# Performance work log

Hardware: AMD Instinct MI355X
Metric: run time of the kernel (lower is better)

## Reference

```python
import jax, jax.numpy as jnp
import numpy as np

DT = 1e-3   # timestep (s)
DH = 10.0   # grid spacing (m)


def setup_inputs() -> dict:
    key = jax.random.key(0)
    k1, k2, k3, k4 = jax.random.split(key, 4)
    B, NT, NZ, NX, NREC = 8, 256, 256, 256, 64
    x = jax.random.normal(k1, (B, NT), dtype=jnp.float32)            # source wavelets
    vp = 1500.0 + 2000.0 * jax.random.uniform(k2, (NZ, NX), dtype=jnp.float32)
    src_loc = jax.random.randint(k3, (B, 2), 4, NZ - 4, dtype=jnp.int32)        # (z,x) per shot
    rec_loc = jax.random.randint(k4, (B, NREC, 2), 4, NZ - 4, dtype=jnp.int32)  # (z,x) per rec
    return {"x": x, "vp": vp, "src_loc": src_loc, "rec_loc": rec_loc}


def reference(x, vp, src_loc, rec_loc):
    """Acoustic 2nd-order leapfrog FD time-stepping (WaveRNN pattern):
    per step: stencil update -> source scatter-inject -> receiver gather.
    Returns receiver traces (B, NT, NREC)."""
    B, NT = x.shape
    nz, nx = vp.shape
    c2dt2 = (vp * vp) * jnp.float32(DT * DT)   # (nz, nx), broadcast over batch
    inv_dh2 = jnp.float32(1.0 / (DH * DH))
    bidx = jnp.arange(B)
    sz, sx = src_loc[:, 0], src_loc[:, 1]
    rz, rx = rec_loc[..., 0], rec_loc[..., 1]

    def laplacian(h):  # 5-point stencil, zero (Dirichlet) boundaries
        interior = (h[:, 2:, 1:-1] + h[:, :-2, 1:-1]
                    + h[:, 1:-1, 2:] + h[:, 1:-1, :-2]
                    - 4.0 * h[:, 1:-1, 1:-1]) * inv_dh2
        return jnp.zeros_like(h).at[:, 1:-1, 1:-1].set(interior)

    def step(carry, wav_t):
        h1, h2 = carry                              # fields at t, t-1
        hn = 2.0 * h1 - h2 + c2dt2 * laplacian(h1)  # leapfrog update
        hn = hn.at[bidx, sz, sx].add(jnp.float32(DT * DT) * wav_t)  # source inject
        rec = hn[bidx[:, None], rz, rx]             # receiver gather (B, NREC)
        return (hn, h1), rec

    h0 = jnp.zeros((B, nz, nx), dtype=x.dtype)
    _, recs = jax.lax.scan(step, (h0, h0), x.T)     # recs: (NT, B, NREC)
    return jnp.transpose(recs, (1, 0, 2))           # (B, NT, NREC)
```

## Files before the change

kernel.cpp:

```cpp
#include <hip/hip_runtime.h>

typedef float v4f __attribute__((ext_vector_type(4)));

namespace {
constexpr int B_     = 8;
constexpr int NT_    = 256;
constexpr int NX_    = 256;
constexpr int NREC_  = 64;
constexpr int PIECES = 32;
constexpr int IROWS  = 8;
constexpr int G      = 16;
constexpr int ROUNDS = NT_ / G;
constexpr int NB     = (IROWS + 2 * G) / 4;
constexpr int NTHR   = NB * 64;
constexpr int NBLK   = B_ * PIECES;
constexpr float DT2  = 1e-6f;
constexpr float KLAP = 1e-8f;
constexpr size_t FLAGS_BYTES = 4096;
constexpr int RCAP = 6;
}

__device__ __forceinline__ float dpp_shr1(float v) {
    return __int_as_float(__builtin_amdgcn_update_dpp(
        0, __float_as_int(v), 0x138 , 0xF, 0xF, true));
}
__device__ __forceinline__ float dpp_shl1(float v) {
    return __int_as_float(__builtin_amdgcn_update_dpp(
        0, __float_as_int(v), 0x130 , 0xF, 0xF, true));
}

__device__ __forceinline__ void store_v4_sys(float* p, v4f v) {
    asm volatile("global_store_dwordx4 %0, %1, off sc0 sc1"
                 :: "v"(p), "v"(v) : "memory");
}
__device__ __forceinline__ v4f load_v4_sys(const float* p) {
    v4f r;
    asm volatile("global_load_dwordx4 %0, %1, off sc0 sc1"
                 : "=v"(r) : "v"(p) : "memory");
    return r;
}

extern "C" __global__
__attribute__((amdgpu_flat_work_group_size(NTHR, NTHR), amdgpu_waves_per_eu(4, 4)))
void wave_reg_kernel(const float* __restrict__ x,
                     const float* __restrict__ vp,
                     const int* __restrict__ src_loc,
                     const int* __restrict__ rec_loc,
                     float* __restrict__ out,
                     int* __restrict__ flags,
                     float* __restrict__ gbuf)
{
    __shared__ float pub[2][2][NB][256];
    __shared__ float wav[NT_];
    __shared__ float recbuf[G][NREC_];
    __shared__ unsigned char recown[NREC_];

    const int bid  = blockIdx.x;
    const int b    = bid & 7;
    const int p    = bid >> 3;
    const int blk  = b * PIECES + p;
    const int tid  = threadIdx.x;
    const int band = tid >> 6;
    const int lane = tid & 63;
    const int c0   = lane << 2;
    const int grt  = p * IROWS - G + (band << 2);

    const int cut = (band < 4) ? ((band << 2) + 3)
                  : ((band < 6) ? G : (39 - (band << 2)));

    if (tid < NT_) wav[tid] = x[b * NT_ + tid];
    if (tid < NREC_) {
        int rz = rec_loc[(b * NREC_ + tid) * 2 + 0];
        recown[tid] = (rz >= p * IROWS && rz < p * IROWS + IROWS) ? 1 : 0;
    }

    v4f cf[4], cf2[4];
#pragma unroll
    for (int i = 0; i < 4; ++i) {
        int gr = grt + i;
        int crow = gr < 0 ? 0 : (gr > 255 ? 255 : gr);
        bool rowok = (gr >= 1) && (gr <= 254);
        v4f vv = *(const v4f*)&vp[crow * NX_ + c0];
        float cc[4];
#pragma unroll
        for (int k = 0; k < 4; ++k) {
            int col = c0 + k;
            float vk = (k == 0) ? vv.x : (k == 1) ? vv.y : (k == 2) ? vv.z : vv.w;
            cc[k] = (rowok && col >= 1 && col <= 254) ? vk * vk * KLAP : 0.f;
        }
        cf[i].x = cc[0]; cf[i].y = cc[1]; cf[i].z = cc[2]; cf[i].w = cc[3];
        cf2[i].x = 2.f - 4.f * cc[0]; cf2[i].y = 2.f - 4.f * cc[1];
        cf2[i].z = 2.f - 4.f * cc[2]; cf2[i].w = 2.f - 4.f * cc[3];
    }

    const int sz = src_loc[b * 2 + 0], sx = src_loc[b * 2 + 1];
    const int si = sz - grt;
    const int sj = sx - c0;
    const bool has_src = ((unsigned)si < 4u) && ((unsigned)sj < 4u);
    const bool wave_has_src = __any(has_src);

    int rs[RCAP]; int rcnt = 0;
#pragma unroll 1
    for (int r = 0; r < NREC_; ++r) {
        int rz = rec_loc[(b * NREC_ + r) * 2 + 0];
        int rx = rec_loc[(b * NREC_ + r) * 2 + 1];
        int i = rz - grt, j = rx - c0;
        if (rz >= p * IROWS && rz < p * IROWS + IROWS &&
            (unsigned)i < 4u && (unsigned)j < 4u) {
            if (rcnt < RCAP) rs[rcnt] = (r << 4) | (i << 2) | j;
            ++rcnt;
        }
    }
    if (rcnt > RCAP) rcnt = RCAP;
    const bool wave_has_rec = __any(rcnt > 0);
    float* outb = out + (size_t)b * NT_ * NREC_;

    v4f A[4], Bv[4];
    {
        v4f z = {0.f, 0.f, 0.f, 0.f};
#pragma unroll
        for (int i = 0; i < 4; ++i) { A[i] = z; Bv[i] = z; }
    }

    auto gptr = [&](int e, int bk, int lvl, int rr) -> float* {
        return gbuf + ((((size_t)(e & 1) * NBLK + bk) * 2 + lvl) * 8 + rr) * 256;
    };

    auto step = [&](v4f (&C)[4], v4f (&P)[4], int t, int par) {
        const int k = (t & (G - 1)) + 1;
        if (k <= cut + 1) {
            *(v4f*)&pub[par][0][band][c0] = C[0];
            *(v4f*)&pub[par][1][band][c0] = C[3];
        }
        __syncthreads();
        if (k > cut) return;
        v4f nn, ss;
        if (band > 0)      nn = *(const v4f*)&pub[par][1][band - 1][c0];
        else               { nn.x = 0.f; nn.y = 0.f; nn.z = 0.f; nn.w = 0.f; }
        if (band < NB - 1) ss = *(const v4f*)&pub[par][0][band + 1][c0];
        else               { ss.x = 0.f; ss.y = 0.f; ss.z = 0.f; ss.w = 0.f; }
#pragma unroll
        for (int i = 0; i < 4; ++i) {
            v4f n = (i == 0) ? nn : C[i - 1];
            v4f s = (i == 3) ? ss : C[i + 1];
            float wv = dpp_shr1(C[i].w);
            float ev = dpp_shl1(C[i].x);
            v4f hn;
            { float sm = (n.x + s.x) + (wv     + C[i].y);
              hn.x = fmaf(cf[i].x, sm, fmaf(cf2[i].x, C[i].x, -P[i].x)); }
            { float sm = (n.y + s.y) + (C[i].x + C[i].z);
              hn.y = fmaf(cf[i].y, sm, fmaf(cf2[i].y, C[i].y, -P[i].y)); }
            { float sm = (n.z + s.z) + (C[i].y + C[i].w);
              hn.z = fmaf(cf[i].z, sm, fmaf(cf2[i].z, C[i].z, -P[i].z)); }
            { float sm = (n.w + s.w) + (C[i].z + ev);
              hn.w = fmaf(cf[i].w, sm, fmaf(cf2[i].w, C[i].w, -P[i].w)); }
            P[i] = hn;
        }
        if (wave_has_src) {
            const float sv = DT2 * wav[t];
#pragma unroll
            for (int i = 0; i < 4; ++i) {
                if (has_src && si == i) {
                    if      (sj == 0) P[i].x += sv;
                    else if (sj == 1) P[i].y += sv;
                    else if (sj == 2) P[i].z += sv;
                    else              P[i].w += sv;
                }
            }
        }
        if (wave_has_rec) {
#pragma unroll
            for (int kk = 0; kk < RCAP; ++kk) {
                if (rcnt > kk) {
                    int pk = rs[kk];
                    int i = (pk >> 2) & 3, j = pk & 3, r = pk >> 4;
                    v4f t01 = (i & 1) ? P[1] : P[0];
                    v4f t23 = (i & 1) ? P[3] : P[2];
                    v4f rw  = (i & 2) ? t23 : t01;
                    float c01 = (j & 1) ? rw.y : rw.x;
                    float c23 = (j & 1) ? rw.w : rw.z;
                    recbuf[t & (G - 1)][r] = (j & 2) ? c23 : c01;
                }
            }
        }
    };

    auto publish_prev = [&](int e) {
        if (band == 4 || band == 5) {
            int rr0 = (band - 4) << 2;
#pragma unroll
            for (int i = 0; i < 4; ++i)
                store_v4_sys(&gptr(e, blk, 1, rr0 + i)[c0], Bv[i]);
        }
    };

    auto exchange = [&](int e) {
        if (band == 4 || band == 5) {
            int rr0 = (band - 4) << 2;
#pragma unroll
            for (int i = 0; i < 4; ++i)
                store_v4_sys(&gptr(e, blk, 0, rr0 + i)[c0], A[i]);
        }
        __syncthreads();
        if (tid == 0)
            __hip_atomic_store(&flags[blk], e + 1, __ATOMIC_RELAXED,
                               __HIP_MEMORY_SCOPE_SYSTEM);
        if (band < 2 && p >= 2) {
            if (lane == 0)
                while (__hip_atomic_load(&flags[blk - 2], __ATOMIC_RELAXED,
                                         __HIP_MEMORY_SCOPE_SYSTEM) < e + 1)
                    __builtin_amdgcn_s_sleep(1);
            int rr0 = band << 2;
#pragma unroll
            for (int i = 0; i < 4; ++i) {
                A[i]  = load_v4_sys(&gptr(e, blk - 2, 0, rr0 + i)[c0]);
                Bv[i] = load_v4_sys(&gptr(e, blk - 2, 1, rr0 + i)[c0]);
            }
        }
        if (band >= 2 && band < 4 && p >= 1) {
            if (lane == 0)
                while (__hip_atomic_load(&flags[blk - 1], __ATOMIC_RELAXED,
                                         __HIP_MEMORY_SCOPE_SYSTEM) < e + 1)
                    __builtin_amdgcn_s_sleep(1);
            int rr0 = (band - 2) << 2;
#pragma unroll
            for (int i = 0; i < 4; ++i) {
                A[i]  = load_v4_sys(&gptr(e, blk - 1, 0, rr0 + i)[c0]);
                Bv[i] = load_v4_sys(&gptr(e, blk - 1, 1, rr0 + i)[c0]);
            }
        }
        if (band >= 6 && band < 8 && p < PIECES - 1) {
            if (lane == 0)
                while (__hip_atomic_load(&flags[blk + 1], __ATOMIC_RELAXED,
                                         __HIP_MEMORY_SCOPE_SYSTEM) < e + 1)
                    __builtin_amdgcn_s_sleep(1);
            int rr0 = (band - 6) << 2;
#pragma unroll
            for (int i = 0; i < 4; ++i) {
                A[i]  = load_v4_sys(&gptr(e, blk + 1, 0, rr0 + i)[c0]);
                Bv[i] = load_v4_sys(&gptr(e, blk + 1, 1, rr0 + i)[c0]);
            }
        }
        if (band >= 8 && p < PIECES - 2) {
            if (lane == 0)
                while (__hip_atomic_load(&flags[blk + 2], __ATOMIC_RELAXED,
                                         __HIP_MEMORY_SCOPE_SYSTEM) < e + 1)
                    __builtin_amdgcn_s_sleep(1);
            int rr0 = (band - 8) << 2;
#pragma unroll
            for (int i = 0; i < 4; ++i) {
                A[i]  = load_v4_sys(&gptr(e, blk + 2, 0, rr0 + i)[c0]);
                Bv[i] = load_v4_sys(&gptr(e, blk + 2, 1, rr0 + i)[c0]);
            }
        }
        asm volatile("s_waitcnt vmcnt(0)" ::: "memory");
        __builtin_amdgcn_sched_barrier(0);
        __syncthreads();
    };

    int t = 0;
#pragma unroll 1
    for (int e = 0; e < ROUNDS; ++e) {
#pragma unroll 1
        for (int s = 0; s < G; s += 2) {
            step(A, Bv, t, 0);
            if (s == G - 2 && e < ROUNDS - 1)
                publish_prev(e);
            step(Bv, A, t + 1, 1);
            t += 2;
        }
        __syncthreads();
#pragma unroll 1
        for (int idx = tid; idx < G * NREC_; idx += NTHR) {
            int s = idx >> 6, r = idx & 63;
            if (recown[r]) outb[(e * G + s) * NREC_ + r] = recbuf[s][r];
        }
        if (e < ROUNDS - 1) exchange(e);
    }
}

extern "C" void kernel_launch(void* const* d_in, const int* in_sizes, int n_in,
                              void* d_out, int out_size, void* d_ws, size_t ws_size,
                              hipStream_t stream) {
    const float* x   = (const float*)d_in[0];
    const float* vp  = (const float*)d_in[1];
    const int*   src = (const int*)d_in[2];
    const int*   rec = (const int*)d_in[3];
    float*       o   = (float*)d_out;
    int*   flags = (int*)d_ws;
    float* gbuf  = (float*)((char*)d_ws + FLAGS_BYTES);
    (void)hipMemsetAsync(d_ws, 0, FLAGS_BYTES, stream);
    hipLaunchKernelGGL(wave_reg_kernel, dim3(NBLK), dim3(NTHR), 0, stream,
                       x, vp, src, rec, o, flags, gbuf);
}
```

Baseline: 298.5 us.

## Widen per-wave bands to eight rows, halving waves per block

Each wave now holds 8 grid rows in registers instead of 4, so a block uses 5 waves instead of 10 to cover the 40-row window of 8 interior rows plus ghost rows. Fewer band boundaries means less LDS halo publishing per step, and barriers synchronize fewer waves. The inner stencil is unrolled by hand, computing interior rows before the halo-dependent edge rows, and the occupancy hint is relaxed to allow more registers. The cost is doubled register pressure per thread and less wave-level parallelism to hide latency. The per-step cutoff schedule is recomputed for the coarser bands.

```diff
diff --git a/kernel.cpp b/kernel.cpp
--- a/kernel.cpp
+++ b/kernel.cpp
@@ -11,8 +11,8 @@
 constexpr int IROWS  = 8;
 constexpr int G      = 16;
 constexpr int ROUNDS = NT_ / G;
-constexpr int NB     = (IROWS + 2 * G) / 4;
-constexpr int NTHR   = NB * 64;
+constexpr int NBANDS = 5;
+constexpr int NTHR   = NBANDS * 64;
 constexpr int NBLK   = B_ * PIECES;
 constexpr float DT2  = 1e-6f;
 constexpr float KLAP = 1e-8f;
@@ -41,7 +41,7 @@
 }
 
 extern "C" __global__
-__attribute__((amdgpu_flat_work_group_size(NTHR, NTHR), amdgpu_waves_per_eu(4, 4)))
+__attribute__((amdgpu_flat_work_group_size(NTHR, NTHR), amdgpu_waves_per_eu(2, 4)))
 void wave_reg_kernel(const float* __restrict__ x,
                      const float* __restrict__ vp,
                      const int* __restrict__ src_loc,
@@ -50,7 +50,7 @@
                      int* __restrict__ flags,
                      float* __restrict__ gbuf)
 {
-    __shared__ float pub[2][2][NB][256];
+    __shared__ float pub[2][2][NBANDS][256];
     __shared__ float wav[NT_];
     __shared__ float recbuf[G][NREC_];
     __shared__ unsigned char recown[NREC_];
@@ -63,10 +63,10 @@
     const int band = tid >> 6;
     const int lane = tid & 63;
     const int c0   = lane << 2;
-    const int grt  = p * IROWS - G + (band << 2);
-
-    const int cut = (band < 4) ? ((band << 2) + 3)
-                  : ((band < 6) ? G : (39 - (band << 2)));
+    const int grt  = p * IROWS - G + (band << 3);
+
+    const int cut = (band < 2) ? ((band << 3) + 7)
+                  : ((band == 2) ? 16 : (((4 - band) << 3) + 7));
 
     if (tid < NT_) wav[tid] = x[b * NT_ + tid];
     if (tid < NREC_) {
@@ -74,9 +74,9 @@
         recown[tid] = (rz >= p * IROWS && rz < p * IROWS + IROWS) ? 1 : 0;
     }
 
-    v4f cf[4], cf2[4];
-#pragma unroll
-    for (int i = 0; i < 4; ++i) {
+    v4f cf[8], cf2[8];
+#pragma unroll
+    for (int i = 0; i < 8; ++i) {
         int gr = grt + i;
         int crow = gr < 0 ? 0 : (gr > 255 ? 255 : gr);
         bool rowok = (gr >= 1) && (gr <= 254);
@@ -96,7 +96,7 @@
     const int sz = src_loc[b * 2 + 0], sx = src_loc[b * 2 + 1];
     const int si = sz - grt;
     const int sj = sx - c0;
-    const bool has_src = ((unsigned)si < 4u) && ((unsigned)sj < 4u);
+    const bool has_src = ((unsigned)si < 8u) && ((unsigned)sj < 4u);
     const bool wave_has_src = __any(has_src);
 
     int rs[RCAP]; int rcnt = 0;
@@ -106,8 +106,8 @@
         int rx = rec_loc[(b * NREC_ + r) * 2 + 1];
         int i = rz - grt, j = rx - c0;
         if (rz >= p * IROWS && rz < p * IROWS + IROWS &&
-            (unsigned)i < 4u && (unsigned)j < 4u) {
-            if (rcnt < RCAP) rs[rcnt] = (r << 4) | (i << 2) | j;
+            (unsigned)i < 8u && (unsigned)j < 4u) {
+            if (rcnt < RCAP) rs[rcnt] = (r << 5) | (i << 2) | j;
             ++rcnt;
         }
     }
@@ -115,51 +115,57 @@
     const bool wave_has_rec = __any(rcnt > 0);
     float* outb = out + (size_t)b * NT_ * NREC_;
 
-    v4f A[4], Bv[4];
+    v4f A[8], Bv[8];
     {
         v4f z = {0.f, 0.f, 0.f, 0.f};
 #pragma unroll
-        for (int i = 0; i < 4; ++i) { A[i] = z; Bv[i] = z; }
+        for (int i = 0; i < 8; ++i) { A[i] = z; Bv[i] = z; }
     }
 
     auto gptr = [&](int e, int bk, int lvl, int rr) -> float* {
         return gbuf + ((((size_t)(e & 1) * NBLK + bk) * 2 + lvl) * 8 + rr) * 256;
     };
 
-    auto step = [&](v4f (&C)[4], v4f (&P)[4], int t, int par) {
+#define ROW(I, NV, SV) do {                                                   \
+    float wv = dpp_shr1(C[I].w);       \
+    float ev = dpp_shl1(C[I].x);      \
+    v4f hn;                                                                   \
+    { float sm = ((NV).x + (SV).x) + (wv     + C[I].y);                       \
+      hn.x = fmaf(cf[I].x, sm, fmaf(cf2[I].x, C[I].x, -P[I].x)); }            \
+    { float sm = ((NV).y + (SV).y) + (C[I].x + C[I].z);                       \
+      hn.y = fmaf(cf[I].y, sm, fmaf(cf2[I].y, C[I].y, -P[I].y)); }            \
+    { float sm = ((NV).z + (SV).z) + (C[I].y + C[I].w);                       \
+      hn.z = fmaf(cf[I].z, sm, fmaf(cf2[I].z, C[I].z, -P[I].z)); }            \
+    { float sm = ((NV).w + (SV).w) + (C[I].z + ev);                           \
+      hn.w = fmaf(cf[I].w, sm, fmaf(cf2[I].w, C[I].w, -P[I].w)); }            \
+    P[I] = hn;                                                                \
+} while (0)
+
+    auto step = [&](v4f (&C)[8], v4f (&P)[8], int t, int par) {
         const int k = (t & (G - 1)) + 1;
         if (k <= cut + 1) {
             *(v4f*)&pub[par][0][band][c0] = C[0];
-            *(v4f*)&pub[par][1][band][c0] = C[3];
+            *(v4f*)&pub[par][1][band][c0] = C[7];
         }
         __syncthreads();
         if (k > cut) return;
         v4f nn, ss;
-        if (band > 0)      nn = *(const v4f*)&pub[par][1][band - 1][c0];
-        else               { nn.x = 0.f; nn.y = 0.f; nn.z = 0.f; nn.w = 0.f; }
-        if (band < NB - 1) ss = *(const v4f*)&pub[par][0][band + 1][c0];
-        else               { ss.x = 0.f; ss.y = 0.f; ss.z = 0.f; ss.w = 0.f; }
-#pragma unroll
-        for (int i = 0; i < 4; ++i) {
-            v4f n = (i == 0) ? nn : C[i - 1];
-            v4f s = (i == 3) ? ss : C[i + 1];
-            float wv = dpp_shr1(C[i].w);
-            float ev = dpp_shl1(C[i].x);
-            v4f hn;
-            { float sm = (n.x + s.x) + (wv     + C[i].y);
-              hn.x = fmaf(cf[i].x, sm, fmaf(cf2[i].x, C[i].x, -P[i].x)); }
-            { float sm = (n.y + s.y) + (C[i].x + C[i].z);
-              hn.y = fmaf(cf[i].y, sm, fmaf(cf2[i].y, C[i].y, -P[i].y)); }
-            { float sm = (n.z + s.z) + (C[i].y + C[i].w);
-              hn.z = fmaf(cf[i].z, sm, fmaf(cf2[i].z, C[i].z, -P[i].z)); }
-            { float sm = (n.w + s.w) + (C[i].z + ev);
-              hn.w = fmaf(cf[i].w, sm, fmaf(cf2[i].w, C[i].w, -P[i].w)); }
-            P[i] = hn;
-        }
+        if (band > 0)          nn = *(const v4f*)&pub[par][1][band - 1][c0];
+        else                   { nn.x = 0.f; nn.y = 0.f; nn.z = 0.f; nn.w = 0.f; }
+        if (band < NBANDS - 1) ss = *(const v4f*)&pub[par][0][band + 1][c0];
+        else                   { ss.x = 0.f; ss.y = 0.f; ss.z = 0.f; ss.w = 0.f; }
+        ROW(1, C[0], C[2]);
+        ROW(2, C[1], C[3]);
+        ROW(3, C[2], C[4]);
+        ROW(4, C[3], C[5]);
+        ROW(5, C[4], C[6]);
+        ROW(6, C[5], C[7]);
+        ROW(0, nn,   C[1]);
+        ROW(7, C[6], ss);
         if (wave_has_src) {
             const float sv = DT2 * wav[t];
 #pragma unroll
-            for (int i = 0; i < 4; ++i) {
+            for (int i = 0; i < 8; ++i) {
                 if (has_src && si == i) {
                     if      (sj == 0) P[i].x += sv;
                     else if (sj == 1) P[i].y += sv;
@@ -173,10 +179,12 @@
             for (int kk = 0; kk < RCAP; ++kk) {
                 if (rcnt > kk) {
                     int pk = rs[kk];
-                    int i = (pk >> 2) & 3, j = pk & 3, r = pk >> 4;
-                    v4f t01 = (i & 1) ? P[1] : P[0];
-                    v4f t23 = (i & 1) ? P[3] : P[2];
-                    v4f rw  = (i & 2) ? t23 : t01;
+                    int i = (pk >> 2) & 7, j = pk & 3, r = pk >> 5;
+                    v4f lo = (i & 2) ? ((i & 1) ? P[3] : P[2])
+                                     : ((i & 1) ? P[1] : P[0]);
+                    v4f hi = (i & 2) ? ((i & 1) ? P[7] : P[6])
+                                     : ((i & 1) ? P[5] : P[4]);
+                    v4f rw = (i & 4) ? hi : lo;
                     float c01 = (j & 1) ? rw.y : rw.x;
                     float c23 = (j & 1) ? rw.w : rw.z;
                     recbuf[t & (G - 1)][r] = (j & 2) ? c23 : c01;
@@ -186,71 +194,65 @@
     };
 
     auto publish_prev = [&](int e) {
-        if (band == 4 || band == 5) {
-            int rr0 = (band - 4) << 2;
-#pragma unroll
-            for (int i = 0; i < 4; ++i)
-                store_v4_sys(&gptr(e, blk, 1, rr0 + i)[c0], Bv[i]);
+        if (band == 2) {
+#pragma unroll
+            for (int i = 0; i < 8; ++i)
+                store_v4_sys(&gptr(e, blk, 1, i)[c0], Bv[i]);
         }
     };
 
     auto exchange = [&](int e) {
-        if (band == 4 || band == 5) {
-            int rr0 = (band - 4) << 2;
-#pragma unroll
-            for (int i = 0; i < 4; ++i)
-                store_v4_sys(&gptr(e, blk, 0, rr0 + i)[c0], A[i]);
+        if (band == 2) {
+#pragma unroll
+            for (int i = 0; i < 8; ++i)
+                store_v4_sys(&gptr(e, blk, 0, i)[c0], A[i]);
         }
         __syncthreads();
         if (tid == 0)
             __hip_atomic_store(&flags[blk], e + 1, __ATOMIC_RELAXED,
                                __HIP_MEMORY_SCOPE_SYSTEM);
-        if (band < 2 && p >= 2) {
+        if (band == 0 && p >= 2) {
             if (lane == 0)
                 while (__hip_atomic_load(&flags[blk - 2], __ATOMIC_RELAXED,
                                          __HIP_MEMORY_SCOPE_SYSTEM) < e + 1)
                     __builtin_amdgcn_s_sleep(1);
-            int rr0 = band << 2;
-#pragma unroll
-            for (int i = 0; i < 4; ++i) {
-                A[i]  = load_v4_sys(&gptr(e, blk - 2, 0, rr0 + i)[c0]);
-                Bv[i] = load_v4_sys(&gptr(e, blk - 2, 1, rr0 + i)[c0]);
-            }
-        }
-        if (band >= 2 && band < 4 && p >= 1) {
+#pragma unroll
+            for (int i = 0; i < 8; ++i) {
+                A[i]  = load_v4_sys(&gptr(e, blk - 2, 0, i)[c0]);
+                Bv[i] = load_v4_sys(&gptr(e, blk - 2, 1, i)[c0]);
+            }
+        }
+        if (band == 1 && p >= 1) {
             if (lane == 0)
                 while (__hip_atomic_load(&flags[blk - 1], __ATOMIC_RELAXED,
                                          __HIP_MEMORY_SCOPE_SYSTEM) < e + 1)
                     __builtin_amdgcn_s_sleep(1);
-            int rr0 = (band - 2) << 2;
-#pragma unroll
-            for (int i = 0; i < 4; ++i) {
-                A[i]  = load_v4_sys(&gptr(e, blk - 1, 0, rr0 + i)[c0]);
-                Bv[i] = load_v4_sys(&gptr(e, blk - 1, 1, rr0 + i)[c0]);
-            }
-        }
-        if (band >= 6 && band < 8 && p < PIECES - 1) {
+#pragma unroll
+            for (int i = 0; i < 8; ++i) {
+                A[i]  = load_v4_sys(&gptr(e, blk - 1, 0, i)[c0]);
+                Bv[i] = load_v4_sys(&gptr(e, blk - 1, 1, i)[c0]);
+            }
+        }
+        if (band == 3 && p < PIECES - 1) {
             if (lane == 0)
                 while (__hip_atomic_load(&flags[blk + 1], __ATOMIC_RELAXED,
                                          __HIP_MEMORY_SCOPE_SYSTEM) < e + 1)
                     __builtin_amdgcn_s_sleep(1);
-            int rr0 = (band - 6) << 2;
-#pragma unroll
-            for (int i = 0; i < 4; ++i) {
-                A[i]  = load_v4_sys(&gptr(e, blk + 1, 0, rr0 + i)[c0]);
-                Bv[i] = load_v4_sys(&gptr(e, blk + 1, 1, rr0 + i)[c0]);
-            }
-        }
-        if (band >= 8 && p < PIECES - 2) {
+#pragma unroll
+            for (int i = 0; i < 8; ++i) {
+                A[i]  = load_v4_sys(&gptr(e, blk + 1, 0, i)[c0]);
+                Bv[i] = load_v4_sys(&gptr(e, blk + 1, 1, i)[c0]);
+            }
+        }
+        if (band == 4 && p < PIECES - 2) {
             if (lane == 0)
                 while (__hip_atomic_load(&flags[blk + 2], __ATOMIC_RELAXED,
                                          __HIP_MEMORY_SCOPE_SYSTEM) < e + 1)
                     __builtin_amdgcn_s_sleep(1);
-            int rr0 = (band - 8) << 2;
-#pragma unroll
-            for (int i = 0; i < 4; ++i) {
-                A[i]  = load_v4_sys(&gptr(e, blk + 2, 0, rr0 + i)[c0]);
-                Bv[i] = load_v4_sys(&gptr(e, blk + 2, 1, rr0 + i)[c0]);
+#pragma unroll
+            for (int i = 0; i < 8; ++i) {
+                A[i]  = load_v4_sys(&gptr(e, blk + 2, 0, i)[c0]);
+                Bv[i] = load_v4_sys(&gptr(e, blk + 2, 1, i)[c0]);
             }
         }
         asm volatile("s_waitcnt vmcnt(0)" ::: "memory");
@@ -277,6 +279,7 @@
         }
         if (e < ROUNDS - 1) exchange(e);
     }
+#undef ROW
 }
 
 extern "C" void kernel_launch(void* const* d_in, const int* in_sizes, int n_in,
```

Result: slower. 310.4 us (+4.0%).

## Fuse two leapfrog steps per barrier using redundant halo-row computation

Applied to the files above, without the earlier changes.

Each band now advances two timesteps per LDS exchange and __syncthreads. It publishes two boundary rows of the current field plus one of the previous field, and recomputes one extra row on each side at the intermediate step. This halves the number of block-wide barriers and LDS round trips in the inner loop. In exchange it adds redundant stencil work for the extra rows, more registers for the wider coefficient arrays (waves_per_eu relaxed to 3), and a larger LDS publish buffer. The publish_prev store is folded into exchange.

```diff
diff --git a/kernel.cpp b/kernel.cpp
--- a/kernel.cpp
+++ b/kernel.cpp
@@ -11,7 +11,7 @@
 constexpr int IROWS  = 8;
 constexpr int G      = 16;
 constexpr int ROUNDS = NT_ / G;
-constexpr int NB     = (IROWS + 2 * G) / 4;
+constexpr int NB     = 10;
 constexpr int NTHR   = NB * 64;
 constexpr int NBLK   = B_ * PIECES;
 constexpr float DT2  = 1e-6f;
@@ -41,7 +41,7 @@
 }
 
 extern "C" __global__
-__attribute__((amdgpu_flat_work_group_size(NTHR, NTHR), amdgpu_waves_per_eu(4, 4)))
+__attribute__((amdgpu_flat_work_group_size(NTHR, NTHR), amdgpu_waves_per_eu(3, 4)))
 void wave_reg_kernel(const float* __restrict__ x,
                      const float* __restrict__ vp,
                      const int* __restrict__ src_loc,
@@ -50,7 +50,7 @@
                      int* __restrict__ flags,
                      float* __restrict__ gbuf)
 {
-    __shared__ float pub[2][2][NB][256];
+    __shared__ float pub[2][NB][6][256];
     __shared__ float wav[NT_];
     __shared__ float recbuf[G][NREC_];
     __shared__ unsigned char recown[NREC_];
@@ -74,10 +74,10 @@
         recown[tid] = (rz >= p * IROWS && rz < p * IROWS + IROWS) ? 1 : 0;
     }
 
-    v4f cf[4], cf2[4];
-#pragma unroll
-    for (int i = 0; i < 4; ++i) {
-        int gr = grt + i;
+    v4f cfx[6], cf2x[6];
+#pragma unroll
+    for (int i = 0; i < 6; ++i) {
+        int gr = grt + i - 1;
         int crow = gr < 0 ? 0 : (gr > 255 ? 255 : gr);
         bool rowok = (gr >= 1) && (gr <= 254);
         v4f vv = *(const v4f*)&vp[crow * NX_ + c0];
@@ -88,16 +88,18 @@
             float vk = (k == 0) ? vv.x : (k == 1) ? vv.y : (k == 2) ? vv.z : vv.w;
             cc[k] = (rowok && col >= 1 && col <= 254) ? vk * vk * KLAP : 0.f;
         }
-        cf[i].x = cc[0]; cf[i].y = cc[1]; cf[i].z = cc[2]; cf[i].w = cc[3];
-        cf2[i].x = 2.f - 4.f * cc[0]; cf2[i].y = 2.f - 4.f * cc[1];
-        cf2[i].z = 2.f - 4.f * cc[2]; cf2[i].w = 2.f - 4.f * cc[3];
+        cfx[i].x = cc[0]; cfx[i].y = cc[1]; cfx[i].z = cc[2]; cfx[i].w = cc[3];
+        cf2x[i].x = 2.f - 4.f * cc[0]; cf2x[i].y = 2.f - 4.f * cc[1];
+        cf2x[i].z = 2.f - 4.f * cc[2]; cf2x[i].w = 2.f - 4.f * cc[3];
     }
 
     const int sz = src_loc[b * 2 + 0], sx = src_loc[b * 2 + 1];
     const int si = sz - grt;
     const int sj = sx - c0;
-    const bool has_src = ((unsigned)si < 4u) && ((unsigned)sj < 4u);
-    const bool wave_has_src = __any(has_src);
+    const bool has_src  = ((unsigned)si < 4u) && ((unsigned)sj < 4u);
+    const bool has_srcx = ((unsigned)(si + 1) < 6u) && ((unsigned)sj < 4u);
+    const bool wave_has_src  = __any(has_src);
+    const bool wave_has_srcx = __any(has_srcx);
 
     int rs[RCAP]; int rcnt = 0;
 #pragma unroll 1
@@ -126,46 +128,81 @@
         return gbuf + ((((size_t)(e & 1) * NBLK + bk) * 2 + lvl) * 8 + rr) * 256;
     };
 
-    auto step = [&](v4f (&C)[4], v4f (&P)[4], int t, int par) {
-        const int k = (t & (G - 1)) + 1;
-        if (k <= cut + 1) {
-            *(v4f*)&pub[par][0][band][c0] = C[0];
-            *(v4f*)&pub[par][1][band][c0] = C[3];
+#define STEN(DST, NV, CV, SV, PV, CI) do {                                    \
+    float wv = dpp_shr1((CV).w);                                              \
+    float ev = dpp_shl1((CV).x);                                              \
+    v4f hn;                                                                   \
+    { float sm = ((NV).x + (SV).x) + (wv     + (CV).y);                       \
+      hn.x = fmaf(cfx[CI].x, sm, fmaf(cf2x[CI].x, (CV).x, -(PV).x)); }        \
+    { float sm = ((NV).y + (SV).y) + ((CV).x + (CV).z);                       \
+      hn.y = fmaf(cfx[CI].y, sm, fmaf(cf2x[CI].y, (CV).y, -(PV).y)); }        \
+    { float sm = ((NV).z + (SV).z) + ((CV).y + (CV).w);                       \
+      hn.z = fmaf(cfx[CI].z, sm, fmaf(cf2x[CI].z, (CV).z, -(PV).z)); }        \
+    { float sm = ((NV).w + (SV).w) + ((CV).z + ev);                           \
+      hn.w = fmaf(cfx[CI].w, sm, fmaf(cf2x[CI].w, (CV).w, -(PV).w)); }        \
+    DST = hn;                                                                 \
+} while (0)
+
+#define INJ(V, SV) do {                                                       \
+    if      (sj == 0) (V).x += (SV);                                          \
+    else if (sj == 1) (V).y += (SV);                                          \
+    else if (sj == 2) (V).z += (SV);                                          \
+    else              (V).w += (SV);                                          \
+} while (0)
+
+    auto fstep = [&](int t, int par) {
+        const int k1 = (t & (G - 1)) + 1;
+        if (k1 - 2 <= cut) {
+            *(v4f*)&pub[par][band][0][c0] = A[0];
+            *(v4f*)&pub[par][band][1][c0] = A[1];
+            *(v4f*)&pub[par][band][2][c0] = Bv[0];
+            *(v4f*)&pub[par][band][3][c0] = A[2];
+            *(v4f*)&pub[par][band][4][c0] = A[3];
+            *(v4f*)&pub[par][band][5][c0] = Bv[3];
         }
         __syncthreads();
-        if (k > cut) return;
-        v4f nn, ss;
-        if (band > 0)      nn = *(const v4f*)&pub[par][1][band - 1][c0];
-        else               { nn.x = 0.f; nn.y = 0.f; nn.z = 0.f; nn.w = 0.f; }
-        if (band < NB - 1) ss = *(const v4f*)&pub[par][0][band + 1][c0];
-        else               { ss.x = 0.f; ss.y = 0.f; ss.z = 0.f; ss.w = 0.f; }
-#pragma unroll
-        for (int i = 0; i < 4; ++i) {
-            v4f n = (i == 0) ? nn : C[i - 1];
-            v4f s = (i == 3) ? ss : C[i + 1];
-            float wv = dpp_shr1(C[i].w);
-            float ev = dpp_shl1(C[i].x);
-            v4f hn;
-            { float sm = (n.x + s.x) + (wv     + C[i].y);
-              hn.x = fmaf(cf[i].x, sm, fmaf(cf2[i].x, C[i].x, -P[i].x)); }
-            { float sm = (n.y + s.y) + (C[i].x + C[i].z);
-              hn.y = fmaf(cf[i].y, sm, fmaf(cf2[i].y, C[i].y, -P[i].y)); }
-            { float sm = (n.z + s.z) + (C[i].y + C[i].w);
-              hn.z = fmaf(cf[i].z, sm, fmaf(cf2[i].z, C[i].z, -P[i].z)); }
-            { float sm = (n.w + s.w) + (C[i].z + ev);
-              hn.w = fmaf(cf[i].w, sm, fmaf(cf2[i].w, C[i].w, -P[i].w)); }
-            P[i] = hn;
-        }
+        if (k1 > cut) return;
+        v4f nC2, nC3, nP3, sC0, sC1, sP0;
+        if (band > 0) {
+            nC2 = *(const v4f*)&pub[par][band - 1][3][c0];
+            nC3 = *(const v4f*)&pub[par][band - 1][4][c0];
+            nP3 = *(const v4f*)&pub[par][band - 1][5][c0];
+        } else { v4f z = {0,0,0,0}; nC2 = z; nC3 = z; nP3 = z; }
+        if (band < NB - 1) {
+            sC0 = *(const v4f*)&pub[par][band + 1][0][c0];
+            sC1 = *(const v4f*)&pub[par][band + 1][1][c0];
+            sP0 = *(const v4f*)&pub[par][band + 1][2][c0];
+        } else { v4f z = {0,0,0,0}; sC0 = z; sC1 = z; sP0 = z; }
+        v4f tm1, t0, t1, t2, t3, t4;
+        STEN(t1, A[0], A[1], A[2], Bv[1], 2);
+        STEN(t2, A[1], A[2], A[3], Bv[2], 3);
+        STEN(t0, nC3, A[0], A[1], Bv[0], 1);
+        STEN(t3, A[2], A[3], sC0, Bv[3], 4);
+        STEN(tm1, nC2, nC3, A[0], nP3, 0);
+        STEN(t4, A[3], sC0, sC1, sP0, 5);
+        if (wave_has_srcx) {
+            const float sv = DT2 * wav[t];
+            if (has_srcx) {
+                if      (si == -1) INJ(tm1, sv);
+                else if (si == 0)  INJ(t0, sv);
+                else if (si == 1)  INJ(t1, sv);
+                else if (si == 2)  INJ(t2, sv);
+                else if (si == 3)  INJ(t3, sv);
+                else               INJ(t4, sv);
+            }
+        }
+        Bv[0] = t0; Bv[1] = t1; Bv[2] = t2; Bv[3] = t3;
+        STEN(A[0], tm1, t0, t1, A[0], 1);
+        STEN(A[1], t0, t1, t2, A[1], 2);
+        STEN(A[2], t1, t2, t3, A[2], 3);
+        STEN(A[3], t2, t3, t4, A[3], 4);
         if (wave_has_src) {
-            const float sv = DT2 * wav[t];
-#pragma unroll
-            for (int i = 0; i < 4; ++i) {
-                if (has_src && si == i) {
-                    if      (sj == 0) P[i].x += sv;
-                    else if (sj == 1) P[i].y += sv;
-                    else if (sj == 2) P[i].z += sv;
-                    else              P[i].w += sv;
-                }
+            const float sv = DT2 * wav[t + 1];
+            if (has_src) {
+                if      (si == 0) INJ(A[0], sv);
+                else if (si == 1) INJ(A[1], sv);
+                else if (si == 2) INJ(A[2], sv);
+                else              INJ(A[3], sv);
             }
         }
         if (wave_has_rec) {
@@ -174,23 +211,20 @@
                 if (rcnt > kk) {
                     int pk = rs[kk];
                     int i = (pk >> 2) & 3, j = pk & 3, r = pk >> 4;
-                    v4f t01 = (i & 1) ? P[1] : P[0];
-                    v4f t23 = (i & 1) ? P[3] : P[2];
-                    v4f rw  = (i & 2) ? t23 : t01;
-                    float c01 = (j & 1) ? rw.y : rw.x;
-                    float c23 = (j & 1) ? rw.w : rw.z;
-                    recbuf[t & (G - 1)][r] = (j & 2) ? c23 : c01;
+                    v4f o01 = (i & 1) ? Bv[1] : Bv[0];
+                    v4f o23 = (i & 1) ? Bv[3] : Bv[2];
+                    v4f ro  = (i & 2) ? o23 : o01;
+                    float oc01 = (j & 1) ? ro.y : ro.x;
+                    float oc23 = (j & 1) ? ro.w : ro.z;
+                    recbuf[t & (G - 1)][r] = (j & 2) ? oc23 : oc01;
+                    v4f e01 = (i & 1) ? A[1] : A[0];
+                    v4f e23 = (i & 1) ? A[3] : A[2];
+                    v4f re  = (i & 2) ? e23 : e01;
+                    float ec01 = (j & 1) ? re.y : re.x;
+                    float ec23 = (j & 1) ? re.w : re.z;
+                    recbuf[(t + 1) & (G - 1)][r] = (j & 2) ? ec23 : ec01;
                 }
             }
-        }
-    };
-
-    auto publish_prev = [&](int e) {
-        if (band == 4 || band == 5) {
-            int rr0 = (band - 4) << 2;
-#pragma unroll
-            for (int i = 0; i < 4; ++i)
-                store_v4_sys(&gptr(e, blk, 1, rr0 + i)[c0], Bv[i]);
         }
     };
 
@@ -198,8 +232,10 @@
         if (band == 4 || band == 5) {
             int rr0 = (band - 4) << 2;
 #pragma unroll
-            for (int i = 0; i < 4; ++i)
+            for (int i = 0; i < 4; ++i) {
                 store_v4_sys(&gptr(e, blk, 0, rr0 + i)[c0], A[i]);
+                store_v4_sys(&gptr(e, blk, 1, rr0 + i)[c0], Bv[i]);
+            }
         }
         __syncthreads();
         if (tid == 0)
@@ -262,11 +298,8 @@
 #pragma unroll 1
     for (int e = 0; e < ROUNDS; ++e) {
 #pragma unroll 1
-        for (int s = 0; s < G; s += 2) {
-            step(A, Bv, t, 0);
-            if (s == G - 2 && e < ROUNDS - 1)
-                publish_prev(e);
-            step(Bv, A, t + 1, 1);
+        for (int c = 0; c < G / 2; ++c) {
+            fstep(t, (t >> 1) & 1);
             t += 2;
         }
         __syncthreads();
@@ -277,6 +310,8 @@
         }
         if (e < ROUNDS - 1) exchange(e);
     }
+#undef STEN
+#undef INJ
 }
 
 extern "C" void kernel_launch(void* const* d_in, const int* in_sizes, int n_in,
```

Result: slower. 311.6 us (+4.4%).
